# Optimization experiments

Measured on AMD Instinct MI355X. Metric: run time of the kernel, lower is better.

The kernel has to match this reference:

```python
import jax, jax.numpy as jnp
import numpy as np

EMBED = 512
HEADS = 8
HD = EMBED // HEADS


def setup_inputs() -> dict:
    key = jax.random.key(0)
    ks = jax.random.split(key, 8)
    N, L = 4, 2048
    queries = jax.random.normal(ks[0], (N, L, EMBED), dtype=jnp.float32)
    keys = jax.random.normal(ks[1], (N, L, EMBED), dtype=jnp.float32)
    values = jax.random.normal(ks[2], (N, L, EMBED), dtype=jnp.float32)
    s = 1.0 / np.sqrt(HD)
    Wq = jax.random.normal(ks[3], (HD, HD), dtype=jnp.float32) * s
    Wk = jax.random.normal(ks[4], (HD, HD), dtype=jnp.float32) * s
    Wv = jax.random.normal(ks[5], (HD, HD), dtype=jnp.float32) * s
    Wo = jax.random.normal(ks[6], (EMBED, EMBED), dtype=jnp.float32) * (1.0 / np.sqrt(EMBED))
    bo = jax.random.normal(ks[7], (EMBED,), dtype=jnp.float32) * 0.01
    return {"queries": queries, "keys": keys, "values": values,
            "Wq": Wq, "Wk": Wk, "Wv": Wv, "Wo": Wo, "bo": bo}


def reference(queries, keys, values, Wq, Wk, Wv, Wo, bo):
    N, Lq, _ = queries.shape
    Lk = keys.shape[1]
    # split heads: [N, L, H, D]
    q = queries.reshape(N, Lq, HEADS, HD)
    k = keys.reshape(N, Lk, HEADS, HD)
    v = values.reshape(N, Lk, HEADS, HD)
    # per-head linear projections (weights shared across heads); torch Linear: x @ W.T
    q = jnp.einsum('nqhd,ed->nqhe', q, Wq)
    k = jnp.einsum('nkhd,ed->nkhe', k, Wk)
    v = jnp.einsum('nkhd,ed->nkhe', v, Wv)
    # scores scaled by sqrt(embed_size) (as in the original, NOT sqrt(head_dim))
    energy = jnp.einsum('nqhd,nkhd->nhqk', q, k) / jnp.sqrt(jnp.float32(EMBED))
    attn = jax.nn.softmax(energy, axis=-1)
    out = jnp.einsum('nhqk,nkhd->nqhd', attn, v).reshape(N, Lq, EMBED)
    return out @ Wo.T + bo
```

## Files before the change

kernel.cpp:

```cpp
#include <hip/hip_runtime.h>
#include <math.h>

#define N_ 4
#define L_ 2048
#define E_ 512
#define H_ 8
#define D_ 64

#define QSCALE 0.06375871588055019f

typedef short s16x8 __attribute__((ext_vector_type(8)));
typedef float f32x4 __attribute__((ext_vector_type(4)));
typedef float f32x16 __attribute__((ext_vector_type(16)));
typedef unsigned int u32x4 __attribute__((ext_vector_type(4)));

typedef const __attribute__((address_space(1))) unsigned int ga_u32;
typedef __attribute__((address_space(3))) unsigned int lds_u32;

__device__ __forceinline__ void gl_lds16(const unsigned short* g, unsigned short* l) {
    __builtin_amdgcn_global_load_lds((ga_u32*)g, (lds_u32*)l, 16, 0, 0);
}
__device__ __forceinline__ float exp2a(float x) {
    float r; asm("v_exp_f32 %0, %1" : "=v"(r) : "v"(x)); return r;
}
__device__ __forceinline__ unsigned int cvtpk(float lo, float hi) {
    unsigned int r; asm("v_cvt_pk_bf16_f32 %0, %1, %2" : "=v"(r) : "v"(lo), "v"(hi)); return r;
}
__device__ __forceinline__ void swap32(unsigned int& a, unsigned int& b) {
    asm volatile("v_permlane32_swap_b32 %0, %1" : "+v"(a), "+v"(b));
}
__device__ __forceinline__ float max3f(float a, float b, float c) {
    return fmaxf(fmaxf(a, b), c);
}
__device__ __forceinline__ unsigned short f2bf(float x) {
    unsigned int u = __builtin_bit_cast(unsigned int, x);
    u = (u + 0x7FFFu + ((u >> 16) & 1u)) >> 16;
    return (unsigned short)u;
}
__device__ __forceinline__ float bflo(unsigned int w) {
    return __builtin_bit_cast(float, w << 16);
}
__device__ __forceinline__ float bfhi(unsigned int w) {
    return __builtin_bit_cast(float, w & 0xFFFF0000u);
}
__device__ __forceinline__ s16x8 ld8(const unsigned short* p) {
    return *reinterpret_cast<const s16x8*>(p);
}

__global__ __launch_bounds__(256) void wo_split_kernel(
    const float* __restrict__ Wo, unsigned short* __restrict__ Whi,
    unsigned short* __restrict__ Wlo)
{
    const int i = blockIdx.x * 256 + threadIdx.x;
    const float4 w = reinterpret_cast<const float4*>(Wo)[i];
    const unsigned int hxy = cvtpk(w.x, w.y);
    const unsigned int hzw = cvtpk(w.z, w.w);
    const unsigned int lxy = cvtpk(w.x - bflo(hxy), w.y - bfhi(hxy));
    const unsigned int lzw = cvtpk(w.z - bflo(hzw), w.w - bfhi(hzw));
    uint2 hh; hh.x = hxy; hh.y = hzw;
    uint2 ll; ll.x = lxy; ll.y = lzw;
    reinterpret_cast<uint2*>(Whi)[i] = hh;
    reinterpret_cast<uint2*>(Wlo)[i] = ll;
}

__global__ __launch_bounds__(256) void qkv_proj_kernel(
    const float* __restrict__ Q, const float* __restrict__ K, const float* __restrict__ V,
    const float* __restrict__ Wq, const float* __restrict__ Wk, const float* __restrict__ Wv,
    unsigned short* __restrict__ Qp, unsigned short* __restrict__ Kp,
    unsigned short* __restrict__ Vt)
{
    __shared__ __align__(16) unsigned short Xl[4096];
    __shared__ __align__(16) unsigned short Whl[4096];
    __shared__ __align__(16) unsigned short Wll[4096];
    __shared__ __align__(16) unsigned short Yl[64][72];

    const int tid = threadIdx.x;
    const int lt = blockIdx.x;
    const int nh = blockIdx.y;
    const int m  = blockIdx.z;
    const int n = nh >> 3, h = nh & 7;
    const int l0 = lt * 64;

    const float* __restrict__ in = (m == 0) ? Q : (m == 1) ? K : V;
    const float* __restrict__ W  = (m == 0) ? Wq : (m == 1) ? Wk : Wv;

    const int xr = tid >> 2;
    const int xc = (tid & 3) * 16;
    {
        const float* xs = in + (size_t)(n * L_ + l0 + xr) * E_ + h * D_ + xc;
        float4 a = reinterpret_cast<const float4*>(xs)[0];
        float4 b = reinterpret_cast<const float4*>(xs)[1];
        float4 c = reinterpret_cast<const float4*>(xs)[2];
        float4 d = reinterpret_cast<const float4*>(xs)[3];
        u32x4 w0, w1;
        w0[0] = cvtpk(a.x, a.y); w0[1] = cvtpk(a.z, a.w);
        w0[2] = cvtpk(b.x, b.y); w0[3] = cvtpk(b.z, b.w);
        w1[0] = cvtpk(c.x, c.y); w1[1] = cvtpk(c.z, c.w);
        w1[2] = cvtpk(d.x, d.y); w1[3] = cvtpk(d.z, d.w);
        const int base  = (xr * 64 + xc) ^ ((xr & 7) << 3);
        const int base2 = (xr * 64 + xc + 8) ^ ((xr & 7) << 3);
        *reinterpret_cast<u32x4*>(&Xl[base])  = w0;
        *reinterpret_cast<u32x4*>(&Xl[base2]) = w1;

        const float* wsrc = W + (size_t)xr * D_ + xc;
        float wv[16];
#pragma unroll
        for (int i = 0; i < 4; ++i) {
            const float4 t = reinterpret_cast<const float4*>(wsrc)[i];
            wv[i * 4 + 0] = t.x; wv[i * 4 + 1] = t.y;
            wv[i * 4 + 2] = t.z; wv[i * 4 + 3] = t.w;
        }
        if (m == 0) {
#pragma unroll
            for (int i = 0; i < 16; ++i) wv[i] *= QSCALE;
        }
        u32x4 hi0, hi1, lo0, lo1;
#pragma unroll
        for (int i = 0; i < 4; ++i) {
            const unsigned int hw = cvtpk(wv[2 * i], wv[2 * i + 1]);
            hi0[i] = hw;
            lo0[i] = cvtpk(wv[2 * i] - bflo(hw), wv[2 * i + 1] - bfhi(hw));
        }
#pragma unroll
        for (int i = 0; i < 4; ++i) {
            const unsigned int hw = cvtpk(wv[8 + 2 * i], wv[8 + 2 * i + 1]);
            hi1[i] = hw;
            lo1[i] = cvtpk(wv[8 + 2 * i] - bflo(hw), wv[8 + 2 * i + 1] - bfhi(hw));
        }
        *reinterpret_cast<u32x4*>(&Whl[base])  = hi0;
        *reinterpret_cast<u32x4*>(&Whl[base2]) = hi1;
        *reinterpret_cast<u32x4*>(&Wll[base])  = lo0;
        *reinterpret_cast<u32x4*>(&Wll[base2]) = lo1;
    }
    __syncthreads();

    const int wave = tid >> 6, lane = tid & 63;
    const int ql = lane & 15, g = lane >> 4;
    const int arow = wave * 16 + ql;

    f32x4 acc[4];
#pragma unroll
    for (int t = 0; t < 4; ++t) acc[t] = (f32x4){0.f, 0.f, 0.f, 0.f};

    if (m < 2) {
        s16x8 xf[2];
#pragma unroll
        for (int ks = 0; ks < 2; ++ks)
            xf[ks] = ld8(&Xl[(arow * 64 + ks * 32 + g * 8) ^ ((arow & 7) << 3)]);
#pragma unroll
        for (int t = 0; t < 4; ++t) {
            const int wrow = t * 16 + ql;
#pragma unroll
            for (int ks = 0; ks < 2; ++ks) {
                const s16x8 bh = ld8(&Whl[(wrow * 64 + ks * 32 + g * 8) ^ ((wrow & 7) << 3)]);
                acc[t] = __builtin_amdgcn_mfma_f32_16x16x32_bf16(xf[ks], bh, acc[t], 0, 0, 0);
                const s16x8 bl = ld8(&Wll[(wrow * 64 + ks * 32 + g * 8) ^ ((wrow & 7) << 3)]);
                acc[t] = __builtin_amdgcn_mfma_f32_16x16x32_bf16(xf[ks], bl, acc[t], 0, 0, 0);
            }
        }
    } else {
        s16x8 whf[2], wlf[2];
#pragma unroll
        for (int ks = 0; ks < 2; ++ks) {
            whf[ks] = ld8(&Whl[(arow * 64 + ks * 32 + g * 8) ^ ((arow & 7) << 3)]);
            wlf[ks] = ld8(&Wll[(arow * 64 + ks * 32 + g * 8) ^ ((arow & 7) << 3)]);
        }
#pragma unroll
        for (int t = 0; t < 4; ++t) {
            const int xrow = t * 16 + ql;
#pragma unroll
            for (int ks = 0; ks < 2; ++ks) {
                const s16x8 bx = ld8(&Xl[(xrow * 64 + ks * 32 + g * 8) ^ ((xrow & 7) << 3)]);
                acc[t] = __builtin_amdgcn_mfma_f32_16x16x32_bf16(whf[ks], bx, acc[t], 0, 0, 0);
                acc[t] = __builtin_amdgcn_mfma_f32_16x16x32_bf16(wlf[ks], bx, acc[t], 0, 0, 0);
            }
        }
    }

#pragma unroll
    for (int t = 0; t < 4; ++t)
#pragma unroll
        for (int r = 0; r < 4; ++r)
            Yl[wave * 16 + g * 4 + r][t * 16 + ql] = f2bf(acc[t][r]);
    __syncthreads();

    const int orow = tid >> 2;
    const int oc = (tid & 3) * 16;
    const uint4 v0 = *reinterpret_cast<const uint4*>(&Yl[orow][oc]);
    const uint4 v1 = *reinterpret_cast<const uint4*>(&Yl[orow][oc + 8]);
    unsigned short* dst;
    if (m == 0)      dst = Qp + ((size_t)nh * L_ + l0 + orow) * D_ + oc;
    else if (m == 1) dst = Kp + ((size_t)nh * L_ + l0 + orow) * D_ + oc;
    else             dst = Vt + ((size_t)nh * D_ + orow) * L_ + l0 + oc;
    *reinterpret_cast<uint4*>(dst) = v0;
    *reinterpret_cast<uint4*>(dst + 8) = v1;
}

__global__ __launch_bounds__(512, 2) void attn_kernel(
    const unsigned short* __restrict__ Qp, const unsigned short* __restrict__ Kp,
    const unsigned short* __restrict__ Vt, unsigned short* __restrict__ AO)
{
    __shared__ __align__(16) unsigned short ST[2][4 * 4096];

    const int tid = threadIdx.x;
    const int phys = blockIdx.x;
    const int bid = (phys & 7) * 64 + (phys >> 3);
    const int qt = bid & 15;
    const int nh = bid >> 4;
    const int n = nh >> 3, h = nh & 7;
    const int q0 = qt * 128;
    const int wave = tid >> 6;
    const int half = wave >> 2;
    const int w4 = wave & 3;
    const int lane = tid & 63;
    const int l31 = lane & 31;
    const int hh  = lane >> 5;

    const unsigned short* __restrict__ Qb = Qp + (size_t)nh * (L_ * D_);
    const unsigned short* __restrict__ Kb = Kp + (size_t)nh * (L_ * D_);
    const unsigned short* __restrict__ Vb = Vt + (size_t)nh * (D_ * L_);

    unsigned short* const Kbuf0 = &ST[half][0];
    unsigned short* const Kbuf1 = &ST[half][4096];
    unsigned short* const Vbuf0 = &ST[half][2 * 4096];
    unsigned short* const Vbuf1 = &ST[half][3 * 4096];

    const int G0 = w4 * 64 + lane;
    const int G1 = G0 + 256;
    const int r0 = G0 >> 3, c0 = (G0 & 7) ^ (r0 & 7);
    const int r1 = G1 >> 3, c1 = (G1 & 7) ^ (r1 & 7);

    const int kbase = half * 1024;
    const unsigned short* ks0 = Kb + (size_t)(kbase + r0) * 64 + c0 * 8;
    const unsigned short* ks1 = Kb + (size_t)(kbase + r1) * 64 + c1 * 8;
    const unsigned short* vs0 = Vb + (size_t)r0 * L_ + kbase + c0 * 8;
    const unsigned short* vs1 = Vb + (size_t)r1 * L_ + kbase + c1 * 8;

    gl_lds16(ks0, Kbuf0 + w4 * 512);
    gl_lds16(ks1, Kbuf0 + 2048 + w4 * 512);
    gl_lds16(vs0, Vbuf0 + w4 * 512);
    gl_lds16(vs1, Vbuf0 + 2048 + w4 * 512);

    const int qrow = q0 + w4 * 32 + l31;
    s16x8 qfrag[4];
#pragma unroll
    for (int ks = 0; ks < 4; ++ks)
        qfrag[ks] = ld8(Qb + (size_t)qrow * D_ + ks * 16 + hh * 8);

    float m_ = -INFINITY;
    float lsum = 0.f;
    f32x16 ot[2];
    ot[0] = (f32x16)0.f;
    ot[1] = (f32x16)0.f;
    s16x8 pf[2];

    const int NS = (L_ / 2) / 32;

    for (int s = 0; s < NS; ++s) {
        const int T = s >> 1;
        if ((s & 1) == 0) {
            __syncthreads();
            if (T + 1 < 16) {
                unsigned short* kn = ((T + 1) & 1) ? Kbuf1 : Kbuf0;
                gl_lds16(ks0 + (T + 1) * 4096, kn + w4 * 512);
                gl_lds16(ks1 + (T + 1) * 4096, kn + 2048 + w4 * 512);
            }
        }
        const unsigned short* __restrict__ Kl = (T & 1) ? Kbuf1 : Kbuf0;
        const int kro = (s & 1) * 32;

        f32x16 st = (f32x16)0.f;
        __builtin_amdgcn_s_setprio(1);
        {
            const int krow = kro + l31;
            const int swz = (l31 & 7) << 3;
#pragma unroll
            for (int ks = 0; ks < 4; ++ks) {
                const s16x8 kf = ld8(&Kl[(krow * 64 + ks * 16 + hh * 8) ^ swz]);
                st = __builtin_amdgcn_mfma_f32_32x32x16_bf16(kf, qfrag[ks], st, 0, 0, 0);
            }
        }

        if (s) {
            const unsigned short* __restrict__ Vl = (((s - 1) >> 1) & 1) ? Vbuf1 : Vbuf0;
            const int vco = ((s - 1) & 1) * 32;
#pragma unroll
            for (int dt = 0; dt < 2; ++dt) {
                const int drow = dt * 32 + l31;
                const int swz = (l31 & 7) << 3;
#pragma unroll
                for (int kc = 0; kc < 2; ++kc) {
                    const s16x8 vf = ld8(&Vl[(drow * 64 + vco + kc * 16 + hh * 8) ^ swz]);
                    ot[dt] = __builtin_amdgcn_mfma_f32_32x32x16_bf16(vf, pf[kc], ot[dt], 0, 0, 0);
                }
            }
        }
        __builtin_amdgcn_s_setprio(0);

        if ((s & 1) == 0) {
            __syncthreads();
            if (T + 1 < 16) {
                unsigned short* vn = ((T + 1) & 1) ? Vbuf1 : Vbuf0;
                gl_lds16(vs0 + (T + 1) * 64, vn + w4 * 512);
                gl_lds16(vs1 + (T + 1) * 64, vn + 2048 + w4 * 512);
            }
        }

        const float t0 = max3f(st[0],  st[1],  st[2]);
        const float t1 = max3f(st[3],  st[4],  st[5]);
        const float t2 = max3f(st[6],  st[7],  st[8]);
        const float t3 = max3f(st[9],  st[10], st[11]);
        const float t4 = max3f(st[12], st[13], st[14]);
        const float u0 = max3f(t0, t1, t2);
        const float u1 = max3f(t3, t4, st[15]);
        float tmax = fmaxf(u0, u1);
        tmax = fmaxf(tmax, __shfl_xor(tmax, 32));

        if (!__all(tmax <= m_ + 8.f)) {
            const float newm = fmaxf(m_, tmax);
            const float corr = exp2a(m_ - newm);
            lsum *= corr;
            ot[0] *= corr;
            ot[1] *= corr;
            m_ = newm;
        }

#pragma unroll
        for (int i = 0; i < 16; ++i) st[i] = exp2a(st[i] - m_);

        {
            float s0 = 0.f, s1 = 0.f, s2 = 0.f, s3 = 0.f;
#pragma unroll
            for (int i = 0; i < 4; ++i) {
                s0 += st[i];      s1 += st[i + 4];
                s2 += st[i + 8];  s3 += st[i + 12];
            }
            float ts = (s0 + s1) + (s2 + s3);
            ts += __shfl_xor(ts, 32);
            lsum += ts;
        }

        {
            unsigned int A0 = cvtpk(st[0],  st[1]),  B0 = cvtpk(st[2],  st[3]);
            unsigned int A1 = cvtpk(st[4],  st[5]),  B1 = cvtpk(st[6],  st[7]);
            unsigned int A2 = cvtpk(st[8],  st[9]),  B2 = cvtpk(st[10], st[11]);
            unsigned int A3 = cvtpk(st[12], st[13]), B3 = cvtpk(st[14], st[15]);
            swap32(A0, A1); swap32(B0, B1);
            swap32(A2, A3); swap32(B2, B3);
            u32x4 lo; lo[0] = A0; lo[1] = B0; lo[2] = A1; lo[3] = B1;
            u32x4 hi; hi[0] = A2; hi[1] = B2; hi[2] = A3; hi[3] = B3;
            pf[0] = __builtin_bit_cast(s16x8, lo);
            pf[1] = __builtin_bit_cast(s16x8, hi);
        }
    }

    {
        const unsigned short* __restrict__ Vl = (((NS - 1) >> 1) & 1) ? Vbuf1 : Vbuf0;
        const int vco = ((NS - 1) & 1) * 32;
        __builtin_amdgcn_s_setprio(1);
#pragma unroll
        for (int dt = 0; dt < 2; ++dt) {
            const int drow = dt * 32 + l31;
            const int swz = (l31 & 7) << 3;
#pragma unroll
            for (int kc = 0; kc < 2; ++kc) {
                const s16x8 vf = ld8(&Vl[(drow * 64 + vco + kc * 16 + hh * 8) ^ swz]);
                ot[dt] = __builtin_amdgcn_mfma_f32_32x32x16_bf16(vf, pf[kc], ot[dt], 0, 0, 0);
            }
        }
        __builtin_amdgcn_s_setprio(0);
    }

    __syncthreads();
    float* mrg = reinterpret_cast<float*>(&ST[0][0]);
    const int slot = ((w4 << 6) + lane) * 36;
    if (half == 1) {
        *reinterpret_cast<f32x16*>(&mrg[slot])      = ot[0];
        *reinterpret_cast<f32x16*>(&mrg[slot + 16]) = ot[1];
        mrg[slot + 32] = m_;
        mrg[slot + 33] = lsum;
    }
    __syncthreads();
    if (half == 0) {
        const f32x16 ob0 = *reinterpret_cast<const f32x16*>(&mrg[slot]);
        const f32x16 ob1 = *reinterpret_cast<const f32x16*>(&mrg[slot + 16]);
        const float mB = mrg[slot + 32];
        const float lB = mrg[slot + 33];
        const float mm = fmaxf(m_, mB);
        const float sA = exp2a(m_ - mm);
        const float sB = exp2a(mB - mm);
        const float inv = 1.f / (lsum * sA + lB * sB);
        ot[0] = ot[0] * sA + ob0 * sB;
        ot[1] = ot[1] * sA + ob1 * sB;

#pragma unroll
        for (int dt = 0; dt < 2; ++dt) {
#pragma unroll
            for (int r = 0; r < 4; ++r) {
                uint2 o;
                o.x = cvtpk(ot[dt][4 * r + 0] * inv, ot[dt][4 * r + 1] * inv);
                o.y = cvtpk(ot[dt][4 * r + 2] * inv, ot[dt][4 * r + 3] * inv);
                const size_t elem = ((size_t)n * L_ + qrow) * E_ + h * D_ + dt * 32 + r * 8 + hh * 4;
                *reinterpret_cast<uint2*>(AO + elem) = o;
            }
        }
    }
}

__global__ __launch_bounds__(256) void out_proj_kernel(
    const unsigned short* __restrict__ AO, const unsigned short* __restrict__ Whi,
    const unsigned short* __restrict__ Wlo, const float* __restrict__ bo,
    float* __restrict__ out)
{
    __shared__ __align__(16) unsigned short Adb[2][4096];
    __shared__ __align__(16) unsigned short Hdb[2][4096];
    __shared__ __align__(16) unsigned short Ldb[2][4096];

    const int tid = threadIdx.x;
    const int bid = blockIdx.x;
    const int mt = bid >> 3, nt = bid & 7;
    const int m0 = mt * 64, n0 = nt * 64;
    const int wave = tid >> 6, lane = tid & 63;
    const int ql = lane & 15, g = lane >> 4;

    const int G0 = wave * 64 + lane;
    const int G1 = G0 + 256;
    const int r0 = G0 >> 3, c0 = (G0 & 7) ^ (r0 & 7);
    const int r1 = G1 >> 3, c1 = (G1 & 7) ^ (r1 & 7);

    const unsigned short* as0 = AO + (size_t)(m0 + r0) * E_ + c0 * 8;
    const unsigned short* as1 = AO + (size_t)(m0 + r1) * E_ + c1 * 8;
    const unsigned short* hs0 = Whi + (size_t)(n0 + r0) * E_ + c0 * 8;
    const unsigned short* hs1 = Whi + (size_t)(n0 + r1) * E_ + c1 * 8;
    const unsigned short* ls0 = Wlo + (size_t)(n0 + r0) * E_ + c0 * 8;
    const unsigned short* ls1 = Wlo + (size_t)(n0 + r1) * E_ + c1 * 8;

    gl_lds16(as0, &Adb[0][wave * 512]);
    gl_lds16(as1, &Adb[0][2048 + wave * 512]);
    gl_lds16(hs0, &Hdb[0][wave * 512]);
    gl_lds16(hs1, &Hdb[0][2048 + wave * 512]);
    gl_lds16(ls0, &Ldb[0][wave * 512]);
    gl_lds16(ls1, &Ldb[0][2048 + wave * 512]);

    float bias[4];
#pragma unroll
    for (int t = 0; t < 4; ++t) bias[t] = bo[n0 + t * 16 + ql];

    f32x4 acc[4];
#pragma unroll
    for (int t = 0; t < 4; ++t) acc[t] = (f32x4){0.f, 0.f, 0.f, 0.f};

    const int arow = wave * 16 + ql;

    for (int kc = 0; kc < 8; ++kc) {
        const int b = kc & 1;
        __syncthreads();
        if (kc + 1 < 8) {
            const int nb = b ^ 1;
            const int ko = (kc + 1) * 64;
            gl_lds16(as0 + ko, &Adb[nb][wave * 512]);
            gl_lds16(as1 + ko, &Adb[nb][2048 + wave * 512]);
            gl_lds16(hs0 + ko, &Hdb[nb][wave * 512]);
            gl_lds16(hs1 + ko, &Hdb[nb][2048 + wave * 512]);
            gl_lds16(ls0 + ko, &Ldb[nb][wave * 512]);
            gl_lds16(ls1 + ko, &Ldb[nb][2048 + wave * 512]);
        }
        const unsigned short* __restrict__ Al = Adb[b];
        const unsigned short* __restrict__ Hl = Hdb[b];
        const unsigned short* __restrict__ Ll = Ldb[b];

        s16x8 af[2];
#pragma unroll
        for (int ks = 0; ks < 2; ++ks)
            af[ks] = ld8(&Al[(arow * 64 + ks * 32 + g * 8) ^ ((arow & 7) << 3)]);

        __builtin_amdgcn_s_setprio(1);
#pragma unroll
        for (int t = 0; t < 4; ++t) {
            const int wrow = t * 16 + ql;
#pragma unroll
            for (int ks = 0; ks < 2; ++ks) {
                const s16x8 bh = ld8(&Hl[(wrow * 64 + ks * 32 + g * 8) ^ ((wrow & 7) << 3)]);
                acc[t] = __builtin_amdgcn_mfma_f32_16x16x32_bf16(af[ks], bh, acc[t], 0, 0, 0);
                const s16x8 bl = ld8(&Ll[(wrow * 64 + ks * 32 + g * 8) ^ ((wrow & 7) << 3)]);
                acc[t] = __builtin_amdgcn_mfma_f32_16x16x32_bf16(af[ks], bl, acc[t], 0, 0, 0);
            }
        }
        __builtin_amdgcn_s_setprio(0);
    }

#pragma unroll
    for (int t = 0; t < 4; ++t) {
#pragma unroll
        for (int r = 0; r < 4; ++r) {
            out[(size_t)(m0 + wave * 16 + g * 4 + r) * E_ + n0 + t * 16 + ql] =
                acc[t][r] + bias[t];
        }
    }
}

extern "C" void kernel_launch(void* const* d_in, const int* in_sizes, int n_in,
                              void* d_out, int out_size, void* d_ws, size_t ws_size,
                              hipStream_t stream)
{
    const float* Q  = (const float*)d_in[0];
    const float* K  = (const float*)d_in[1];
    const float* V  = (const float*)d_in[2];
    const float* Wq = (const float*)d_in[3];
    const float* Wk = (const float*)d_in[4];
    const float* Wv = (const float*)d_in[5];
    const float* Wo = (const float*)d_in[6];
    const float* bo = (const float*)d_in[7];
    float* out = (float*)d_out;

    unsigned short* ws = (unsigned short*)d_ws;
    const size_t SZ = (size_t)N_ * H_ * L_ * D_;
    unsigned short* Qp  = ws;
    unsigned short* Kp  = ws + SZ;
    unsigned short* Vt  = ws + 2 * SZ;
    unsigned short* AO  = ws + 3 * SZ;
    unsigned short* Whi = ws + 4 * SZ;
    unsigned short* Wlo = ws + 4 * SZ + 262144;

    qkv_proj_kernel<<<dim3(32, 32, 3), 256, 0, stream>>>(Q, K, V, Wq, Wk, Wv, Qp, Kp, Vt);
    wo_split_kernel<<<256, 256, 0, stream>>>(Wo, Whi, Wlo);
    attn_kernel<<<512, 512, 0, stream>>>(Qp, Kp, Vt, AO);
    out_proj_kernel<<<(8192 / 64) * (E_ / 64), 256, 0, stream>>>(AO, Whi, Wlo, bo, out);
}
```

Before: 91.10 us.

## Fold Wo split into QKV kernel and compute softmax row sums via MFMA

The separate Wo hi/lo split kernel is removed and its work runs as an extra z-slice of the QKV projection grid, saving one kernel launch. In the attention kernel, the per-step VALU reduction and cross-lane shuffle for the softmax denominator are replaced by extra MFMAs that multiply the bf16 probabilities by a ones matrix. This moves work off the VALU onto the matrix unit, but adds two MFMAs per step and a 16-register accumulator. The denominator is now summed from bf16-rounded probabilities, which matches the values actually used in the PV product. The extra grid slice launches 1024 blocks of which only 256 do work.

```diff
diff --git a/kernel.cpp b/kernel.cpp
--- a/kernel.cpp
+++ b/kernel.cpp
@@ -47,27 +47,13 @@
     return *reinterpret_cast<const s16x8*>(p);
 }
 
-__global__ __launch_bounds__(256) void wo_split_kernel(
-    const float* __restrict__ Wo, unsigned short* __restrict__ Whi,
-    unsigned short* __restrict__ Wlo)
-{
-    const int i = blockIdx.x * 256 + threadIdx.x;
-    const float4 w = reinterpret_cast<const float4*>(Wo)[i];
-    const unsigned int hxy = cvtpk(w.x, w.y);
-    const unsigned int hzw = cvtpk(w.z, w.w);
-    const unsigned int lxy = cvtpk(w.x - bflo(hxy), w.y - bfhi(hxy));
-    const unsigned int lzw = cvtpk(w.z - bflo(hzw), w.w - bfhi(hzw));
-    uint2 hh; hh.x = hxy; hh.y = hzw;
-    uint2 ll; ll.x = lxy; ll.y = lzw;
-    reinterpret_cast<uint2*>(Whi)[i] = hh;
-    reinterpret_cast<uint2*>(Wlo)[i] = ll;
-}
-
 __global__ __launch_bounds__(256) void qkv_proj_kernel(
     const float* __restrict__ Q, const float* __restrict__ K, const float* __restrict__ V,
     const float* __restrict__ Wq, const float* __restrict__ Wk, const float* __restrict__ Wv,
+    const float* __restrict__ Wo,
     unsigned short* __restrict__ Qp, unsigned short* __restrict__ Kp,
-    unsigned short* __restrict__ Vt)
+    unsigned short* __restrict__ Vt,
+    unsigned short* __restrict__ Whi, unsigned short* __restrict__ Wlo)
 {
     __shared__ __align__(16) unsigned short Xl[4096];
     __shared__ __align__(16) unsigned short Whl[4096];
@@ -80,6 +66,23 @@
     const int m  = blockIdx.z;
     const int n = nh >> 3, h = nh & 7;
     const int l0 = lt * 64;
+
+    if (m == 3) {
+        const int bidx = lt + nh * 32;
+        if (bidx < 256) {
+            const int i = bidx * 256 + tid;
+            const float4 w = reinterpret_cast<const float4*>(Wo)[i];
+            const unsigned int hxy = cvtpk(w.x, w.y);
+            const unsigned int hzw = cvtpk(w.z, w.w);
+            const unsigned int lxy = cvtpk(w.x - bflo(hxy), w.y - bfhi(hxy));
+            const unsigned int lzw = cvtpk(w.z - bflo(hzw), w.w - bfhi(hzw));
+            uint2 hh2; hh2.x = hxy; hh2.y = hzw;
+            uint2 ll2; ll2.x = lxy; ll2.y = lzw;
+            reinterpret_cast<uint2*>(Whi)[i] = hh2;
+            reinterpret_cast<uint2*>(Wlo)[i] = ll2;
+        }
+        return;
+    }
 
     const float* __restrict__ in = (m == 0) ? Q : (m == 1) ? K : V;
     const float* __restrict__ W  = (m == 0) ? Wq : (m == 1) ? Wk : Wv;
@@ -247,8 +250,12 @@
     for (int ks = 0; ks < 4; ++ks)
         qfrag[ks] = ld8(Qb + (size_t)qrow * D_ + ks * 16 + hh * 8);
 
+    s16x8 onesf;
+#pragma unroll
+    for (int i = 0; i < 8; ++i) onesf[i] = (short)0x3F80;
+
     float m_ = -INFINITY;
-    float lsum = 0.f;
+    f32x16 lsacc = (f32x16)0.f;
     f32x16 ot[2];
     ot[0] = (f32x16)0.f;
     ot[1] = (f32x16)0.f;
@@ -294,6 +301,9 @@
                     ot[dt] = __builtin_amdgcn_mfma_f32_32x32x16_bf16(vf, pf[kc], ot[dt], 0, 0, 0);
                 }
             }
+#pragma unroll
+            for (int kc = 0; kc < 2; ++kc)
+                lsacc = __builtin_amdgcn_mfma_f32_32x32x16_bf16(onesf, pf[kc], lsacc, 0, 0, 0);
         }
         __builtin_amdgcn_s_setprio(0);
 
@@ -319,7 +329,7 @@
         if (!__all(tmax <= m_ + 8.f)) {
             const float newm = fmaxf(m_, tmax);
             const float corr = exp2a(m_ - newm);
-            lsum *= corr;
+            lsacc *= corr;
             ot[0] *= corr;
             ot[1] *= corr;
             m_ = newm;
@@ -327,18 +337,6 @@
 
 #pragma unroll
         for (int i = 0; i < 16; ++i) st[i] = exp2a(st[i] - m_);
-
-        {
-            float s0 = 0.f, s1 = 0.f, s2 = 0.f, s3 = 0.f;
-#pragma unroll
-            for (int i = 0; i < 4; ++i) {
-                s0 += st[i];      s1 += st[i + 4];
-                s2 += st[i + 8];  s3 += st[i + 12];
-            }
-            float ts = (s0 + s1) + (s2 + s3);
-            ts += __shfl_xor(ts, 32);
-            lsum += ts;
-        }
 
         {
             unsigned int A0 = cvtpk(st[0],  st[1]),  B0 = cvtpk(st[2],  st[3]);
@@ -368,6 +366,9 @@
                 ot[dt] = __builtin_amdgcn_mfma_f32_32x32x16_bf16(vf, pf[kc], ot[dt], 0, 0, 0);
             }
         }
+#pragma unroll
+        for (int kc = 0; kc < 2; ++kc)
+            lsacc = __builtin_amdgcn_mfma_f32_32x32x16_bf16(onesf, pf[kc], lsacc, 0, 0, 0);
         __builtin_amdgcn_s_setprio(0);
     }
 
@@ -378,7 +379,7 @@
         *reinterpret_cast<f32x16*>(&mrg[slot])      = ot[0];
         *reinterpret_cast<f32x16*>(&mrg[slot + 16]) = ot[1];
         mrg[slot + 32] = m_;
-        mrg[slot + 33] = lsum;
+        mrg[slot + 33] = lsacc[0];
     }
     __syncthreads();
     if (half == 0) {
@@ -389,7 +390,7 @@
         const float mm = fmaxf(m_, mB);
         const float sA = exp2a(m_ - mm);
         const float sB = exp2a(mB - mm);
-        const float inv = 1.f / (lsum * sA + lB * sB);
+        const float inv = 1.f / (lsacc[0] * sA + lB * sB);
         ot[0] = ot[0] * sA + ob0 * sB;
         ot[1] = ot[1] * sA + ob1 * sB;
 
@@ -522,8 +523,8 @@
     unsigned short* Whi = ws + 4 * SZ;
     unsigned short* Wlo = ws + 4 * SZ + 262144;
 
-    qkv_proj_kernel<<<dim3(32, 32, 3), 256, 0, stream>>>(Q, K, V, Wq, Wk, Wv, Qp, Kp, Vt);
-    wo_split_kernel<<<256, 256, 0, stream>>>(Wo, Whi, Wlo);
+    qkv_proj_kernel<<<dim3(32, 32, 4), 256, 0, stream>>>(Q, K, V, Wq, Wk, Wv, Wo,
+                                                         Qp, Kp, Vt, Whi, Wlo);
     attn_kernel<<<512, 512, 0, stream>>>(Qp, Kp, Vt, AO);
     out_proj_kernel<<<(8192 / 64) * (E_ / 64), 256, 0, stream>>>(AO, Whi, Wlo, bo, out);
 }
```

Measured after the change: 89.09 us. 1.02x faster.
